# Optimization experiments

Hardware: AMD Instinct MI355X
Metric: run time of the kernel (lower is better)

Reference implementation:

```python
import math
import jax, jax.numpy as jnp
import numpy as np

B, T, C, H = 4, 2048, 1024, 16
D = C // H  # head dim = 64


def setup_inputs() -> dict:
    key = jax.random.key(0)
    ks = jax.random.split(key, 9)
    s = 1.0 / math.sqrt(C)
    return {
        "x": jax.random.normal(ks[0], (B, T, C), jnp.float32),
        "Wq": jax.random.normal(ks[1], (C, C), jnp.float32) * s,
        "bq": jax.random.normal(ks[2], (C,), jnp.float32) * 0.02,
        "Wk": jax.random.normal(ks[3], (C, C), jnp.float32) * s,
        "bk": jax.random.normal(ks[4], (C,), jnp.float32) * 0.02,
        "Wv": jax.random.normal(ks[5], (C, C), jnp.float32) * s,
        "bv": jax.random.normal(ks[6], (C,), jnp.float32) * 0.02,
        "Wo": jax.random.normal(ks[7], (C, C), jnp.float32) * s,
        "bo": jax.random.normal(ks[8], (C,), jnp.float32) * 0.02,
    }


def reference(x, Wq, bq, Wk, bk, Wv, bv, Wo, bo):
    # Projections: (B,T,C) -> (B,H,T,D)
    def heads(y):
        return y.reshape(B, T, H, D).transpose(0, 2, 1, 3)

    q = heads(x @ Wq + bq)
    k = heads(x @ Wk + bk)
    v = heads(x @ Wv + bv)

    scale = 1.0 / math.sqrt(D)
    scores = jnp.einsum("bhqd,bhkd->bhqk", q, k) * scale  # (B,H,T,T)
    causal = jnp.tril(jnp.ones((T, T), dtype=bool))
    scores = jnp.where(causal[None, None], scores, jnp.float32(-jnp.inf))
    att = jax.nn.softmax(scores, axis=-1)

    y = jnp.einsum("bhqk,bhkd->bhqd", att, v)  # (B,H,T,D)
    y = y.transpose(0, 2, 1, 3).reshape(B, T, C)
    return y @ Wo + bo
```

## Files before the change

kernel.cpp:

```cpp
#include <hip/hip_runtime.h>

#define B_ 4
#define T_ 2048
#define C_ 1024
#define H_ 16
#define D_ 64
#define M_ (B_*T_)
#define CR3 3072

typedef unsigned short u16;
typedef __attribute__((ext_vector_type(8))) short short8;
typedef __attribute__((ext_vector_type(8))) unsigned short ushort8_t;
typedef __attribute__((ext_vector_type(4))) unsigned short ushort4_t;
typedef __attribute__((ext_vector_type(4))) float floatx4;
typedef __attribute__((ext_vector_type(16))) float f32x16;
typedef __attribute__((ext_vector_type(4))) unsigned int uint4_t;

__device__ __forceinline__ u16 f2bf(float f) {
  union { float f; unsigned u; } v; v.f = f;
  unsigned r = v.u + 0x7fffu + ((v.u >> 16) & 1u);
  return (u16)(r >> 16);
}

__device__ __forceinline__ void gload16(const void* g, void* l) {
  __builtin_amdgcn_global_load_lds((__attribute__((address_space(1))) void*)(g),
                                   (__attribute__((address_space(3))) void*)(l),
                                   16, 0, 0);
}

__device__ __forceinline__ unsigned cvtpk(float lo, float hi) {
  unsigned r;
  asm("v_cvt_pk_bf16_f32 %0, %1, %2" : "=v"(r) : "v"(lo), "v"(hi));
  return r;
}

__device__ __forceinline__ void pl32swap(unsigned &a, unsigned &b) {
  asm volatile("v_permlane32_swap_b32 %0, %1" : "+v"(a), "+v"(b));
}

#define MFMA32(a, b, c) __builtin_amdgcn_mfma_f32_32x32x16_bf16(a, b, c, 0, 0, 0)
#define MFMA16(a, b, c) __builtin_amdgcn_mfma_f32_16x16x32_bf16(a, b, c, 0, 0, 0)

__global__ __launch_bounds__(256) void convx_k(const float* __restrict__ x,
                                               u16* __restrict__ o) {
  int i = (blockIdx.x * 256 + threadIdx.x) * 4;
  floatx4 v = *(const floatx4*)(x + i);
  ushort4_t r;
#pragma unroll
  for (int j = 0; j < 4; ++j) r[j] = f2bf(v[j]);
  *(ushort4_t*)(o + i) = r;
}

__global__ __launch_bounds__(256) void wconv_k(const float* __restrict__ W0,
                                               const float* __restrict__ W1,
                                               const float* __restrict__ W2,
                                               const float* __restrict__ W3,
                                               u16* __restrict__ WT) {
  __shared__ float tile[64][65];
  const float* W = blockIdx.z == 0 ? W0 : blockIdx.z == 1 ? W1 : blockIdx.z == 2 ? W2 : W3;
  const float sc = blockIdx.z == 0 ? 0.125f * 1.44269504f : 1.0f;
  u16* Wt = WT + (size_t)blockIdx.z * (C_ * C_);
  int k0 = blockIdx.x * 64, n0 = blockIdx.y * 64;
  int t = threadIdx.x;
  int r = t >> 2, c0 = (t & 3) * 16;
#pragma unroll
  for (int j = 0; j < 4; ++j) {
    floatx4 v = *(const floatx4*)(W + (size_t)(k0 + r) * C_ + n0 + c0 + j * 4);
#pragma unroll
    for (int jj = 0; jj < 4; ++jj) tile[r][c0 + j * 4 + jj] = v[jj];
  }
  __syncthreads();
  ushort8_t o0, o1;
#pragma unroll
  for (int j = 0; j < 8; ++j) o0[j] = f2bf(tile[c0 + j][r] * sc);
#pragma unroll
  for (int j = 0; j < 8; ++j) o1[j] = f2bf(tile[c0 + 8 + j][r] * sc);
  *(ushort8_t*)(Wt + (size_t)(n0 + r) * C_ + k0 + c0) = o0;
  *(ushort8_t*)(Wt + (size_t)(n0 + r) * C_ + k0 + c0 + 8) = o1;
}

__global__ __launch_bounds__(256, 2) void gemm8_k(const u16* __restrict__ A,
                                                  const u16* __restrict__ Wt,
                                                  const float* __restrict__ b0,
                                                  const float* __restrict__ b1,
                                                  const float* __restrict__ b2,
                                                  float bsc0,
                                                  u16* __restrict__ Cout) {
  __shared__ u16 lds3[36864];
  const int tid = threadIdx.x;
  const int lane = tid & 63, wn = tid >> 6;
  const int l15 = lane & 15, g = lane >> 4;

  const int bid = blockIdx.x;
  const int swz = (bid & 7) * 96 + (bid >> 3);
  const int bn = swz >> 6, bm = swz & 63;
  const int m0 = bm * 128, n0 = bn * 256;

  const int srow = tid >> 2;
  const int scol = ((tid & 3) ^ ((srow >> 1) & 3)) * 8;
  const u16* gA = A  + (size_t)(m0 + srow) * 1024 + scol;
  const u16* gB = Wt + (size_t)(n0 + srow) * 1024 + scol;

#define STAGE(KT) do { \
    u16* s_ = lds3 + ((KT) % 3) * 12288; \
    gload16(gA + (KT) * 32,                      s_ + tid * 8); \
    gload16(gA + (size_t)64 * 1024 + (KT) * 32,  s_ + 2048 + tid * 8); \
    gload16(gB + (KT) * 32,                      s_ + 4096 + tid * 8); \
    gload16(gB + (size_t)64 * 1024 + (KT) * 32,  s_ + 6144 + tid * 8); \
    gload16(gB + (size_t)128 * 1024 + (KT) * 32, s_ + 8192 + tid * 8); \
    gload16(gB + (size_t)192 * 1024 + (KT) * 32, s_ + 10240 + tid * 8); \
  } while (0)

  floatx4 acc[8][4] = {};

  STAGE(0);
  STAGE(1);

  for (int kt = 0; kt < 32; ++kt) {
    if (kt < 31) asm volatile("s_waitcnt vmcnt(6)" ::: "memory");
    else         asm volatile("s_waitcnt vmcnt(0)" ::: "memory");
    __builtin_amdgcn_s_barrier();
    __builtin_amdgcn_sched_barrier(0);
    if (kt < 30) STAGE(kt + 2);

    const u16* Ab = lds3 + (kt % 3) * 12288;
    const u16* Bb = Ab + 4096;
    short8 af[8], bf[4];
#pragma unroll
    for (int mi = 0; mi < 8; ++mi) {
      int ra = mi * 16 + l15;
      af[mi] = *(const short8*)(Ab + ra * 32 + ((g ^ ((ra >> 1) & 3)) << 3));
    }
#pragma unroll
    for (int ni = 0; ni < 4; ++ni) {
      int rb = wn * 64 + ni * 16 + l15;
      bf[ni] = *(const short8*)(Bb + rb * 32 + ((g ^ ((rb >> 1) & 3)) << 3));
    }
    __builtin_amdgcn_s_setprio(1);
#pragma unroll
    for (int mi = 0; mi < 8; ++mi)
#pragma unroll
      for (int ni = 0; ni < 4; ++ni)
        acc[mi][ni] = MFMA16(af[mi], bf[ni], acc[mi][ni]);
    __builtin_amdgcn_s_setprio(0);
  }

#pragma unroll
  for (int mi = 0; mi < 8; ++mi) {
    int row = m0 + mi * 16 + g * 4;
#pragma unroll
    for (int ni = 0; ni < 4; ++ni) {
      int col = n0 + wn * 64 + ni * 16 + l15;
      int seg = col >> 10;
      const float* bp = seg == 0 ? b0 : seg == 1 ? b1 : b2;
      float bv = bp[col & 1023] * (seg == 0 ? bsc0 : 1.0f);
#pragma unroll
      for (int i = 0; i < 4; ++i)
        Cout[(size_t)(row + i) * CR3 + col] = f2bf(acc[mi][ni][i] + bv);
    }
  }
}

template <int OUTF32>
__global__ __launch_bounds__(256, 2) void gemm_k(const u16* __restrict__ A,
                                                 int astride,
                                                 const u16* __restrict__ Wt,
                                                 const float* __restrict__ b0,
                                                 void* __restrict__ Cout, int ostride) {
  __shared__ u16 As[128 * 32];
  __shared__ u16 Bs[128 * 32];
  const int tid = threadIdx.x;
  const int w = tid >> 6, lane = tid & 63;
  const int wr = (w >> 1) * 64, wc = (w & 1) * 64;
  const int l15 = lane & 15, g = lane >> 4;
  const int m0 = blockIdx.x * 128, n0 = blockIdx.y * 128;

  floatx4 acc[4][4] = {};

  const int srow = tid >> 2;
  const int scol = ((tid & 3) ^ ((srow >> 1) & 3)) * 8;
  const u16* ga = A + (size_t)(m0 + srow) * astride + scol;
  const u16* gb = Wt + (size_t)(n0 + srow) * C_ + scol;
  u16* lA = As + tid * 8;
  u16* lB = Bs + tid * 8;

  for (int kt = 0; kt < C_; kt += 32) {
    gload16(ga + kt, lA);
    gload16(ga + kt + (size_t)64 * astride, lA + 64 * 32);
    gload16(gb + kt, lB);
    gload16(gb + kt + (size_t)64 * C_, lB + 64 * 32);
    asm volatile("s_waitcnt vmcnt(0)" ::: "memory");
    __syncthreads();
    short8 af[4], bf[4];
#pragma unroll
    for (int i = 0; i < 4; ++i) {
      int ra = wr + i * 16 + l15;
      af[i] = *(const short8*)(As + ra * 32 + ((g ^ ((ra >> 1) & 3)) << 3));
    }
#pragma unroll
    for (int i = 0; i < 4; ++i) {
      int rb = wc + i * 16 + l15;
      bf[i] = *(const short8*)(Bs + rb * 32 + ((g ^ ((rb >> 1) & 3)) << 3));
    }
#pragma unroll
    for (int mi = 0; mi < 4; ++mi)
#pragma unroll
      for (int ni = 0; ni < 4; ++ni)
        acc[mi][ni] = MFMA16(af[mi], bf[ni], acc[mi][ni]);
    __syncthreads();
  }
#pragma unroll
  for (int mi = 0; mi < 4; ++mi) {
    int row = m0 + wr + mi * 16 + g * 4;
#pragma unroll
    for (int ni = 0; ni < 4; ++ni) {
      int col = n0 + wc + ni * 16 + l15;
      float bv = b0[col];
#pragma unroll
      for (int i = 0; i < 4; ++i) {
        float v = acc[mi][ni][i] + bv;
        if (OUTF32)
          ((float*)Cout)[(size_t)(row + i) * ostride + col] = v;
        else
          ((u16*)Cout)[(size_t)(row + i) * ostride + col] = f2bf(v);
      }
    }
  }
}

__global__ __launch_bounds__(256, 2) void attn_k(const u16* __restrict__ QKV,
                                                 u16* __restrict__ Yg) {
  __shared__ u16 Ks[2][64 * 64];
  __shared__ u16 Vt[2][64 * 64];

  const int tid = threadIdx.x;
  const int w = tid >> 6, lane = tid & 63;
  const int qi = lane & 31, h = lane >> 5;

  const int lid = blockIdx.x;
  const int a4 = lid >> 6;
  const int gq = a4 >> 2, iq = a4 & 3;
  const int jt = gq == 0 ? 15 - 2 * iq : gq == 1 ? 2 * iq : gq == 2 ? 14 - 2 * iq : 1 + 2 * iq;
  const int bh = lid & 63;
  const int nt = 2 * jt + 2;

  const size_t baseQ = (size_t)(bh >> 4) * T_ * CR3 + (size_t)(bh & 15) * D_;
  const size_t baseY = (size_t)(bh >> 4) * T_ * C_ + (size_t)(bh & 15) * D_;
  const u16* Kg = QKV + baseQ + 1024;
  const u16* Vg = QKV + baseQ + 2048;

  const int srow = tid >> 3, schunk = tid & 7;
  const int sgcol = (schunk ^ (srow & 7)) * 8;
  const u16* Kgr = Kg + (size_t)srow * CR3 + sgcol;
  const u16* Vgr = Vg + (size_t)srow * CR3 + schunk * 8;

  const int qw0 = 128 * jt + 32 * w;
  const int q_abs = qw0 + qi;

  short8 qf0, qf1, qf2, qf3;
  {
    const u16* Qr = QKV + baseQ + (size_t)q_abs * CR3 + 8 * h;
    qf0 = *(const short8*)(Qr);      qf1 = *(const short8*)(Qr + 16);
    qf2 = *(const short8*)(Qr + 32); qf3 = *(const short8*)(Qr + 48);
  }

  ushort8_t va, vbr;
  gload16(Kgr, &Ks[0][tid * 8]);
  gload16(Kgr + (size_t)32 * CR3, &Ks[0][2048 + tid * 8]);
  va = *(const ushort8_t*)(Vgr);
  vbr = *(const ushort8_t*)(Vgr + (size_t)32 * CR3);

  f32x16 y0 = {}, y1 = {};
  float l_run = 0.f;
  const float M0 = 13.0f;

  for (int t = 0; t < nt; ++t) {
    const int kv0 = t * 64;
    u16* Kb = Ks[t & 1];
    u16* Vb = Vt[t & 1];
    asm volatile("s_waitcnt vmcnt(0)" ::: "memory");
    {
      char* vbp = (char*)Vb;
#pragma unroll
      for (int j = 0; j < 8; ++j) {
        int d = schunk * 8 + j;
        int sl = ((schunk ^ j) & 7) << 4;
        *(u16*)(vbp + d * 128 + ((2 * srow) ^ sl)) = va[j];
        *(u16*)(vbp + d * 128 + ((2 * (srow + 32)) ^ sl)) = vbr[j];
      }
    }
    __syncthreads();
    if (t + 1 < nt) {
      int nkv = (t + 1) * 64;
      u16* dst = Ks[(t + 1) & 1];
      gload16(Kgr + (size_t)nkv * CR3, dst + tid * 8);
      gload16(Kgr + (size_t)(nkv + 32) * CR3, dst + 2048 + tid * 8);
      va = *(const ushort8_t*)(Vgr + (size_t)nkv * CR3);
      vbr = *(const ushort8_t*)(Vgr + (size_t)(nkv + 32) * CR3);
    }

    if (kv0 <= qw0 + 31) {
      f32x16 s0 = {}, s1 = {};
      {
        const int swq = (qi & 7) << 4;
        const char* kr0 = (const char*)Kb + qi * 128;
        const char* kr1 = (const char*)Kb + (qi + 32) * 128;
        short8 k0, k1;
        k0 = *(const short8*)(kr0 + ((16 * h) ^ swq));
        k1 = *(const short8*)(kr1 + ((16 * h) ^ swq));
        s0 = MFMA32(k0, qf0, s0); s1 = MFMA32(k1, qf0, s1);
        k0 = *(const short8*)(kr0 + ((32 + 16 * h) ^ swq));
        k1 = *(const short8*)(kr1 + ((32 + 16 * h) ^ swq));
        s0 = MFMA32(k0, qf1, s0); s1 = MFMA32(k1, qf1, s1);
        k0 = *(const short8*)(kr0 + ((64 + 16 * h) ^ swq));
        k1 = *(const short8*)(kr1 + ((64 + 16 * h) ^ swq));
        s0 = MFMA32(k0, qf2, s0); s1 = MFMA32(k1, qf2, s1);
        k0 = *(const short8*)(kr0 + ((96 + 16 * h) ^ swq));
        k1 = *(const short8*)(kr1 + ((96 + 16 * h) ^ swq));
        s0 = MFMA32(k0, qf3, s0); s1 = MFMA32(k1, qf3, s1);
      }
      if (kv0 + 63 > qw0) {
#pragma unroll
        for (int r = 0; r < 16; ++r) {
          int kvq = (r & 3) + 8 * (r >> 2) + 4 * h;
          if (kv0 + kvq > q_abs) s0[r] = -1e30f;
          if (kv0 + 32 + kvq > q_abs) s1[r] = -1e30f;
        }
      }
#pragma unroll
      for (int r = 0; r < 16; ++r) s0[r] = __builtin_amdgcn_exp2f(s0[r] - M0);
#pragma unroll
      for (int r = 0; r < 16; ++r) s1[r] = __builtin_amdgcn_exp2f(s1[r] - M0);
      {
        float a8[8];
#pragma unroll
        for (int r = 0; r < 8; ++r) a8[r] = (s0[r] + s0[r + 8]) + (s1[r] + s1[r + 8]);
#pragma unroll
        for (int r = 0; r < 4; ++r) a8[r] += a8[r + 4];
        l_run += (a8[0] + a8[1]) + (a8[2] + a8[3]);
      }
      unsigned pw[16];
      {
        unsigned a0, b0, a1, b1;
        a0 = cvtpk(s0[0], s0[1]);  b0 = cvtpk(s0[4], s0[5]);  pl32swap(a0, b0);
        a1 = cvtpk(s0[2], s0[3]);  b1 = cvtpk(s0[6], s0[7]);  pl32swap(a1, b1);
        pw[0] = a0; pw[1] = a1; pw[2] = b0; pw[3] = b1;
        a0 = cvtpk(s0[8], s0[9]);  b0 = cvtpk(s0[12], s0[13]); pl32swap(a0, b0);
        a1 = cvtpk(s0[10], s0[11]); b1 = cvtpk(s0[14], s0[15]); pl32swap(a1, b1);
        pw[4] = a0; pw[5] = a1; pw[6] = b0; pw[7] = b1;
        a0 = cvtpk(s1[0], s1[1]);  b0 = cvtpk(s1[4], s1[5]);  pl32swap(a0, b0);
        a1 = cvtpk(s1[2], s1[3]);  b1 = cvtpk(s1[6], s1[7]);  pl32swap(a1, b1);
        pw[8] = a0; pw[9] = a1; pw[10] = b0; pw[11] = b1;
        a0 = cvtpk(s1[8], s1[9]);  b0 = cvtpk(s1[12], s1[13]); pl32swap(a0, b0);
        a1 = cvtpk(s1[10], s1[11]); b1 = cvtpk(s1[14], s1[15]); pl32swap(a1, b1);
        pw[12] = a0; pw[13] = a1; pw[14] = b0; pw[15] = b1;
      }
      {
        const char* vb0 = (const char*)Vb + qi * 128;
        const char* vb1 = (const char*)Vb + (qi + 32) * 128;
        const int sx0 = (((qi >> 3) ^ qi) & 7) << 4;
        const int sx1 = sx0 ^ 0x40;
#pragma unroll
        for (int c = 0; c < 4; ++c) {
          int cb = 32 * c + 16 * h;
          uint4_t pt = {pw[c * 4 + 0], pw[c * 4 + 1], pw[c * 4 + 2], pw[c * 4 + 3]};
          short8 pa = __builtin_bit_cast(short8, pt);
          short8 v0 = *(const short8*)(vb0 + (cb ^ sx0));
          short8 v1 = *(const short8*)(vb1 + (cb ^ sx1));
          y0 = MFMA32(pa, v0, y0);
          y1 = MFMA32(pa, v1, y1);
        }
      }
    }
  }

  l_run += __shfl_xor(l_run, 32);
  float linv = 1.0f / l_run;
#pragma unroll
  for (int r = 0; r < 16; ++r) {
    int qp = (r & 3) + 8 * (r >> 2) + 4 * h;
    float lv = __shfl(linv, qp);
    size_t row = baseY + (size_t)(qw0 + qp) * C_;
    Yg[row + qi] = f2bf(y0[r] * lv);
    Yg[row + 32 + qi] = f2bf(y1[r] * lv);
  }
}

extern "C" void kernel_launch(void* const* d_in, const int* in_sizes, int n_in,
                              void* d_out, int out_size, void* d_ws, size_t ws_size,
                              hipStream_t stream) {
  const float* x  = (const float*)d_in[0];
  const float* Wq = (const float*)d_in[1];
  const float* bq = (const float*)d_in[2];
  const float* Wk = (const float*)d_in[3];
  const float* bk = (const float*)d_in[4];
  const float* Wv = (const float*)d_in[5];
  const float* bv = (const float*)d_in[6];
  const float* Wo = (const float*)d_in[7];
  const float* bo = (const float*)d_in[8];
  float* out = (float*)d_out;

  char* ws = (char*)d_ws;
  u16* xb   = (u16*)ws;
  u16* WT   = (u16*)(ws + (size_t)16777216);
  u16* QKVb = (u16*)(ws + (size_t)25165824);
  u16* Yb = xb;

  convx_k<<<dim3(M_ * C_ / 1024), 256, 0, stream>>>(x, xb);
  wconv_k<<<dim3(16, 16, 4), 256, 0, stream>>>(Wq, Wk, Wv, Wo, WT);
  gemm8_k<<<dim3(768), 256, 0, stream>>>(xb, WT, bq, bk, bv, 0.125f * 1.44269504f, QKVb);
  attn_k<<<dim3(1024), 256, 0, stream>>>(QKVb, Yb);
  gemm_k<1><<<dim3(64, 8), 256, 0, stream>>>(Yb, C_, WT + (size_t)3 * 1048576, bo, out, C_);
}
```

Baseline: 163.7 us.

## Restructure QKV GEMM into 256x256 tiles with 8-wave phased pipeline

The QKV projection GEMM moves from 128x256 tiles with 4 waves and a 3-stage ring buffer to 256x256 tiles with 8 waves, K-steps of 64, and a double-buffered LDS schedule. Global loads are interleaved into eight compute phases per iteration, each bracketed by barriers. Larger tiles increase operand reuse and halve the grid. The cost is 128KB of LDS per block, which limits occupancy, plus more barriers. The attention kernel also wraps its MFMA pairs in s_setprio to favour matrix issue.

```diff
diff --git a/kernel.cpp b/kernel.cpp
--- a/kernel.cpp
+++ b/kernel.cpp
@@ -79,75 +79,94 @@
   *(ushort8_t*)(Wt + (size_t)(n0 + r) * C_ + k0 + c0 + 8) = o1;
 }
 
-__global__ __launch_bounds__(256, 2) void gemm8_k(const u16* __restrict__ A,
+__global__ __launch_bounds__(512, 2) void gemm8_k(const u16* __restrict__ A,
                                                   const u16* __restrict__ Wt,
                                                   const float* __restrict__ b0,
                                                   const float* __restrict__ b1,
                                                   const float* __restrict__ b2,
                                                   float bsc0,
                                                   u16* __restrict__ Cout) {
-  __shared__ u16 lds3[36864];
+  __shared__ u16 lds[65536];
   const int tid = threadIdx.x;
-  const int lane = tid & 63, wn = tid >> 6;
+  const int lane = tid & 63, w = tid >> 6;
+  const int wm = w >> 2, wn = w & 3;
   const int l15 = lane & 15, g = lane >> 4;
 
   const int bid = blockIdx.x;
-  const int swz = (bid & 7) * 96 + (bid >> 3);
-  const int bn = swz >> 6, bm = swz & 63;
-  const int m0 = bm * 128, n0 = bn * 256;
-
-  const int srow = tid >> 2;
-  const int scol = ((tid & 3) ^ ((srow >> 1) & 3)) * 8;
-  const u16* gA = A  + (size_t)(m0 + srow) * 1024 + scol;
-  const u16* gB = Wt + (size_t)(n0 + srow) * 1024 + scol;
-
-#define STAGE(KT) do { \
-    u16* s_ = lds3 + ((KT) % 3) * 12288; \
-    gload16(gA + (KT) * 32,                      s_ + tid * 8); \
-    gload16(gA + (size_t)64 * 1024 + (KT) * 32,  s_ + 2048 + tid * 8); \
-    gload16(gB + (KT) * 32,                      s_ + 4096 + tid * 8); \
-    gload16(gB + (size_t)64 * 1024 + (KT) * 32,  s_ + 6144 + tid * 8); \
-    gload16(gB + (size_t)128 * 1024 + (KT) * 32, s_ + 8192 + tid * 8); \
-    gload16(gB + (size_t)192 * 1024 + (KT) * 32, s_ + 10240 + tid * 8); \
+  const int swz = (bid & 7) * 48 + (bid >> 3);
+  const int bn = swz >> 5, bm = swz & 31;
+  const int m0 = bm * 256, n0 = bn * 256;
+
+  const int srow = tid >> 3;
+  const int scol = ((tid & 7) ^ (srow & 7)) * 8;
+  const u16* gAsrc = A  + (size_t)(m0 + srow) * 1024 + scol;
+  const u16* gBsrc = Wt + (size_t)(n0 + srow) * 1024 + scol;
+
+#define SQA(DD, Q, KT) gload16(gAsrc + (size_t)(Q) * 65536 + (size_t)(KT) * 64, \
+                               lds + (DD) * 32768 + (Q) * 4096 + tid * 8)
+#define SQB(DD, Q, KT) gload16(gBsrc + (size_t)(Q) * 65536 + (size_t)(KT) * 64, \
+                               lds + (DD) * 32768 + 16384 + (Q) * 4096 + tid * 8)
+
+  floatx4 acc[8][4] = {};
+  short8 bk0[4], bk1[4];
+
+#define PHASE(DD, MH, KS, READB, BKREG, STG, VM) do {                       \
+    short8 af_[4];                                                          \
+    _Pragma("unroll") for (int mi = 0; mi < 4; ++mi) {                      \
+      int ar_ = wm * 128 + (MH) * 64 + mi * 16 + l15;                       \
+      af_[mi] = *(const short8*)(lds + (DD) * 32768 + ar_ * 64 +            \
+                                 ((((KS) * 4 + g) ^ (ar_ & 7)) << 3));      \
+    }                                                                       \
+    if (READB) {                                                            \
+      _Pragma("unroll") for (int ni = 0; ni < 4; ++ni) {                    \
+        int br_ = wn * 64 + ni * 16 + l15;                                  \
+        BKREG[ni] = *(const short8*)(lds + (DD) * 32768 + 16384 + br_ * 64 +\
+                                     ((((KS) * 4 + g) ^ (br_ & 7)) << 3));  \
+      }                                                                     \
+    }                                                                       \
+    STG;                                                                    \
+    VM;                                                                     \
+    __builtin_amdgcn_s_barrier();                                           \
+    asm volatile("s_waitcnt lgkmcnt(0)" ::: "memory");                      \
+    __builtin_amdgcn_sched_barrier(0);                                      \
+    __builtin_amdgcn_s_setprio(1);                                          \
+    _Pragma("unroll") for (int mi = 0; mi < 4; ++mi)                        \
+      _Pragma("unroll") for (int ni = 0; ni < 4; ++ni)                      \
+        acc[(MH) * 4 + mi][ni] = MFMA16(af_[mi], BKREG[ni],                 \
+                                        acc[(MH) * 4 + mi][ni]);            \
+    __builtin_amdgcn_s_setprio(0);                                          \
+    __builtin_amdgcn_sched_barrier(0);                                      \
+    __builtin_amdgcn_s_barrier();                                           \
   } while (0)
 
-  floatx4 acc[8][4] = {};
-
-  STAGE(0);
-  STAGE(1);
-
-  for (int kt = 0; kt < 32; ++kt) {
-    if (kt < 31) asm volatile("s_waitcnt vmcnt(6)" ::: "memory");
-    else         asm volatile("s_waitcnt vmcnt(0)" ::: "memory");
-    __builtin_amdgcn_s_barrier();
-    __builtin_amdgcn_sched_barrier(0);
-    if (kt < 30) STAGE(kt + 2);
-
-    const u16* Ab = lds3 + (kt % 3) * 12288;
-    const u16* Bb = Ab + 4096;
-    short8 af[8], bf[4];
-#pragma unroll
-    for (int mi = 0; mi < 8; ++mi) {
-      int ra = mi * 16 + l15;
-      af[mi] = *(const short8*)(Ab + ra * 32 + ((g ^ ((ra >> 1) & 3)) << 3));
-    }
-#pragma unroll
-    for (int ni = 0; ni < 4; ++ni) {
-      int rb = wn * 64 + ni * 16 + l15;
-      bf[ni] = *(const short8*)(Bb + rb * 32 + ((g ^ ((rb >> 1) & 3)) << 3));
-    }
-    __builtin_amdgcn_s_setprio(1);
-#pragma unroll
-    for (int mi = 0; mi < 8; ++mi)
-#pragma unroll
-      for (int ni = 0; ni < 4; ++ni)
-        acc[mi][ni] = MFMA16(af[mi], bf[ni], acc[mi][ni]);
-    __builtin_amdgcn_s_setprio(0);
-  }
-
-#pragma unroll
-  for (int mi = 0; mi < 8; ++mi) {
-    int row = m0 + mi * 16 + g * 4;
+#define VM4 asm volatile("s_waitcnt vmcnt(4)" ::: "memory")
+#define VM0 asm volatile("s_waitcnt vmcnt(0)" ::: "memory")
+#define NOP ((void)0)
+
+  SQA(0, 0, 0); SQA(0, 1, 0); SQA(0, 2, 0); SQA(0, 3, 0);
+  SQB(0, 0, 0); SQB(0, 1, 0); SQB(0, 2, 0); SQB(0, 3, 0);
+  SQB(1, 0, 1); SQB(1, 1, 1); SQB(1, 2, 1); SQB(1, 3, 1);
+  VM4;
+  __builtin_amdgcn_s_barrier();
+
+  for (int i = 0; i < 8; ++i) {
+    const int t1 = 2 * i + 1, T2 = 2 * i + 2, T3 = 2 * i + 3;
+    const bool st = (i < 7);
+    PHASE(0, 0, 0, 1, bk0, { SQA(1, 0, t1); SQA(1, 1, t1); }, NOP);
+    PHASE(0, 0, 1, 1, bk1, { SQA(1, 2, t1); SQA(1, 3, t1); }, NOP);
+    PHASE(0, 1, 0, 0, bk0, { if (st) { SQB(0, 0, T2); SQB(0, 1, T2); } }, NOP);
+    if (st) { PHASE(0, 1, 1, 0, bk1, { SQB(0, 2, T2); SQB(0, 3, T2); }, VM4); }
+    else    { PHASE(0, 1, 1, 0, bk1, NOP, VM0); }
+    PHASE(1, 0, 0, 1, bk0, { if (st) { SQA(0, 0, T2); SQA(0, 1, T2); } }, NOP);
+    PHASE(1, 0, 1, 1, bk1, { if (st) { SQA(0, 2, T2); SQA(0, 3, T2); } }, NOP);
+    PHASE(1, 1, 0, 0, bk0, { if (st) { SQB(1, 0, T3); SQB(1, 1, T3); } }, NOP);
+    if (st) { PHASE(1, 1, 1, 0, bk1, { SQB(1, 2, T3); SQB(1, 3, T3); }, VM4); }
+    else    { PHASE(1, 1, 1, 0, bk1, NOP, VM0); }
+  }
+
+#pragma unroll
+  for (int mi8 = 0; mi8 < 8; ++mi8) {
+    int row = m0 + wm * 128 + mi8 * 16 + g * 4;
 #pragma unroll
     for (int ni = 0; ni < 4; ++ni) {
       int col = n0 + wn * 64 + ni * 16 + l15;
@@ -156,7 +175,7 @@
       float bv = bp[col & 1023] * (seg == 0 ? bsc0 : 1.0f);
 #pragma unroll
       for (int i = 0; i < 4; ++i)
-        Cout[(size_t)(row + i) * CR3 + col] = f2bf(acc[mi][ni][i] + bv);
+        Cout[(size_t)(row + i) * CR3 + col] = f2bf(acc[mi8][ni][i] + bv);
     }
   }
 }
@@ -308,16 +327,24 @@
         short8 k0, k1;
         k0 = *(const short8*)(kr0 + ((16 * h) ^ swq));
         k1 = *(const short8*)(kr1 + ((16 * h) ^ swq));
+        __builtin_amdgcn_s_setprio(1);
         s0 = MFMA32(k0, qf0, s0); s1 = MFMA32(k1, qf0, s1);
+        __builtin_amdgcn_s_setprio(0);
         k0 = *(const short8*)(kr0 + ((32 + 16 * h) ^ swq));
         k1 = *(const short8*)(kr1 + ((32 + 16 * h) ^ swq));
+        __builtin_amdgcn_s_setprio(1);
         s0 = MFMA32(k0, qf1, s0); s1 = MFMA32(k1, qf1, s1);
+        __builtin_amdgcn_s_setprio(0);
         k0 = *(const short8*)(kr0 + ((64 + 16 * h) ^ swq));
         k1 = *(const short8*)(kr1 + ((64 + 16 * h) ^ swq));
+        __builtin_amdgcn_s_setprio(1);
         s0 = MFMA32(k0, qf2, s0); s1 = MFMA32(k1, qf2, s1);
+        __builtin_amdgcn_s_setprio(0);
         k0 = *(const short8*)(kr0 + ((96 + 16 * h) ^ swq));
         k1 = *(const short8*)(kr1 + ((96 + 16 * h) ^ swq));
+        __builtin_amdgcn_s_setprio(1);
         s0 = MFMA32(k0, qf3, s0); s1 = MFMA32(k1, qf3, s1);
+        __builtin_amdgcn_s_setprio(0);
       }
       if (kv0 + 63 > qw0) {
 #pragma unroll
@@ -367,8 +394,10 @@
           short8 pa = __builtin_bit_cast(short8, pt);
           short8 v0 = *(const short8*)(vb0 + (cb ^ sx0));
           short8 v1 = *(const short8*)(vb1 + (cb ^ sx1));
+          __builtin_amdgcn_s_setprio(1);
           y0 = MFMA32(pa, v0, y0);
           y1 = MFMA32(pa, v1, y1);
+          __builtin_amdgcn_s_setprio(0);
         }
       }
     }
@@ -408,7 +437,7 @@
 
   convx_k<<<dim3(M_ * C_ / 1024), 256, 0, stream>>>(x, xb);
   wconv_k<<<dim3(16, 16, 4), 256, 0, stream>>>(Wq, Wk, Wv, Wo, WT);
-  gemm8_k<<<dim3(768), 256, 0, stream>>>(xb, WT, bq, bk, bv, 0.125f * 1.44269504f, QKVb);
+  gemm8_k<<<dim3(384), 512, 0, stream>>>(xb, WT, bq, bk, bv, 0.125f * 1.44269504f, QKVb);
   attn_k<<<dim3(1024), 256, 0, stream>>>(QKVb, Yb);
   gemm_k<1><<<dim3(64, 8), 256, 0, stream>>>(Yb, C_, WT + (size_t)3 * 1048576, bo, out, C_);
 }
```

After: 163.2 us. About the same (-0.3%).

## Rewrite output projection GEMM with 3-stage LDS pipeline and larger tiles

Applied to the files above, without the earlier changes.

Replaces the generic output-projection GEMM with a specialised kernel that uses 128x256 tiles, a triple-buffered LDS pipeline with partial vmcnt waits, and a swizzled block order for L2 locality. Each wave now computes 8x4 MFMA tiles, sharing the A tile across all waves. The intent is to overlap global loads with MFMA work and drop the per-iteration double barrier of the old kernel. It also adds s_setprio around MFMA groups in the attention kernel to favour matrix issue. The larger accumulator and 72KB of LDS may limit occupancy.

```diff
diff --git a/kernel.cpp b/kernel.cpp
--- a/kernel.cpp
+++ b/kernel.cpp
@@ -161,69 +161,79 @@
   }
 }
 
-template <int OUTF32>
-__global__ __launch_bounds__(256, 2) void gemm_k(const u16* __restrict__ A,
-                                                 int astride,
-                                                 const u16* __restrict__ Wt,
-                                                 const float* __restrict__ b0,
-                                                 void* __restrict__ Cout, int ostride) {
-  __shared__ u16 As[128 * 32];
-  __shared__ u16 Bs[128 * 32];
+__global__ __launch_bounds__(256, 2) void gemmO_k(const u16* __restrict__ A,
+                                                  const u16* __restrict__ Wt,
+                                                  const float* __restrict__ b0,
+                                                  float* __restrict__ Cout) {
+  __shared__ u16 lds3[36864];
   const int tid = threadIdx.x;
-  const int w = tid >> 6, lane = tid & 63;
-  const int wr = (w >> 1) * 64, wc = (w & 1) * 64;
+  const int lane = tid & 63, wn = tid >> 6;
   const int l15 = lane & 15, g = lane >> 4;
-  const int m0 = blockIdx.x * 128, n0 = blockIdx.y * 128;
-
-  floatx4 acc[4][4] = {};
+
+  const int bid = blockIdx.x;
+  const int swz = (bid & 7) * 32 + (bid >> 3);
+  const int bn = swz >> 6, bm = swz & 63;
+  const int m0 = bm * 128, n0 = bn * 256;
 
   const int srow = tid >> 2;
   const int scol = ((tid & 3) ^ ((srow >> 1) & 3)) * 8;
-  const u16* ga = A + (size_t)(m0 + srow) * astride + scol;
-  const u16* gb = Wt + (size_t)(n0 + srow) * C_ + scol;
-  u16* lA = As + tid * 8;
-  u16* lB = Bs + tid * 8;
-
-  for (int kt = 0; kt < C_; kt += 32) {
-    gload16(ga + kt, lA);
-    gload16(ga + kt + (size_t)64 * astride, lA + 64 * 32);
-    gload16(gb + kt, lB);
-    gload16(gb + kt + (size_t)64 * C_, lB + 64 * 32);
-    asm volatile("s_waitcnt vmcnt(0)" ::: "memory");
-    __syncthreads();
-    short8 af[4], bf[4];
-#pragma unroll
-    for (int i = 0; i < 4; ++i) {
-      int ra = wr + i * 16 + l15;
-      af[i] = *(const short8*)(As + ra * 32 + ((g ^ ((ra >> 1) & 3)) << 3));
-    }
-#pragma unroll
-    for (int i = 0; i < 4; ++i) {
-      int rb = wc + i * 16 + l15;
-      bf[i] = *(const short8*)(Bs + rb * 32 + ((g ^ ((rb >> 1) & 3)) << 3));
-    }
-#pragma unroll
-    for (int mi = 0; mi < 4; ++mi)
+  const u16* gA = A  + (size_t)(m0 + srow) * 1024 + scol;
+  const u16* gB = Wt + (size_t)(n0 + srow) * 1024 + scol;
+
+#define STAGEO(KT) do { \
+    u16* s_ = lds3 + ((KT) % 3) * 12288; \
+    gload16(gA + (KT) * 32,                      s_ + tid * 8); \
+    gload16(gA + (size_t)64 * 1024 + (KT) * 32,  s_ + 2048 + tid * 8); \
+    gload16(gB + (KT) * 32,                      s_ + 4096 + tid * 8); \
+    gload16(gB + (size_t)64 * 1024 + (KT) * 32,  s_ + 6144 + tid * 8); \
+    gload16(gB + (size_t)128 * 1024 + (KT) * 32, s_ + 8192 + tid * 8); \
+    gload16(gB + (size_t)192 * 1024 + (KT) * 32, s_ + 10240 + tid * 8); \
+  } while (0)
+
+  floatx4 acc[8][4] = {};
+
+  STAGEO(0);
+  STAGEO(1);
+
+  for (int kt = 0; kt < 32; ++kt) {
+    if (kt < 31) asm volatile("s_waitcnt vmcnt(6)" ::: "memory");
+    else         asm volatile("s_waitcnt vmcnt(0)" ::: "memory");
+    __builtin_amdgcn_s_barrier();
+    __builtin_amdgcn_sched_barrier(0);
+    if (kt < 30) STAGEO(kt + 2);
+
+    const u16* Ab = lds3 + (kt % 3) * 12288;
+    const u16* Bb = Ab + 4096;
+    short8 af[8], bf[4];
+#pragma unroll
+    for (int mi = 0; mi < 8; ++mi) {
+      int ra = mi * 16 + l15;
+      af[mi] = *(const short8*)(Ab + ra * 32 + ((g ^ ((ra >> 1) & 3)) << 3));
+    }
+#pragma unroll
+    for (int ni = 0; ni < 4; ++ni) {
+      int rb = wn * 64 + ni * 16 + l15;
+      bf[ni] = *(const short8*)(Bb + rb * 32 + ((g ^ ((rb >> 1) & 3)) << 3));
+    }
+    __builtin_amdgcn_s_setprio(1);
+#pragma unroll
+    for (int mi = 0; mi < 8; ++mi)
 #pragma unroll
       for (int ni = 0; ni < 4; ++ni)
         acc[mi][ni] = MFMA16(af[mi], bf[ni], acc[mi][ni]);
-    __syncthreads();
-  }
-#pragma unroll
-  for (int mi = 0; mi < 4; ++mi) {
-    int row = m0 + wr + mi * 16 + g * 4;
+    __builtin_amdgcn_s_setprio(0);
+  }
+
+#pragma unroll
+  for (int mi = 0; mi < 8; ++mi) {
+    int row = m0 + mi * 16 + g * 4;
 #pragma unroll
     for (int ni = 0; ni < 4; ++ni) {
-      int col = n0 + wc + ni * 16 + l15;
+      int col = n0 + wn * 64 + ni * 16 + l15;
       float bv = b0[col];
 #pragma unroll
-      for (int i = 0; i < 4; ++i) {
-        float v = acc[mi][ni][i] + bv;
-        if (OUTF32)
-          ((float*)Cout)[(size_t)(row + i) * ostride + col] = v;
-        else
-          ((u16*)Cout)[(size_t)(row + i) * ostride + col] = f2bf(v);
-      }
+      for (int i = 0; i < 4; ++i)
+        Cout[(size_t)(row + i) * 1024 + col] = acc[mi][ni][i] + bv;
     }
   }
 }
@@ -308,16 +318,24 @@
         short8 k0, k1;
         k0 = *(const short8*)(kr0 + ((16 * h) ^ swq));
         k1 = *(const short8*)(kr1 + ((16 * h) ^ swq));
+        __builtin_amdgcn_s_setprio(1);
         s0 = MFMA32(k0, qf0, s0); s1 = MFMA32(k1, qf0, s1);
+        __builtin_amdgcn_s_setprio(0);
         k0 = *(const short8*)(kr0 + ((32 + 16 * h) ^ swq));
         k1 = *(const short8*)(kr1 + ((32 + 16 * h) ^ swq));
+        __builtin_amdgcn_s_setprio(1);
         s0 = MFMA32(k0, qf1, s0); s1 = MFMA32(k1, qf1, s1);
+        __builtin_amdgcn_s_setprio(0);
         k0 = *(const short8*)(kr0 + ((64 + 16 * h) ^ swq));
         k1 = *(const short8*)(kr1 + ((64 + 16 * h) ^ swq));
+        __builtin_amdgcn_s_setprio(1);
         s0 = MFMA32(k0, qf2, s0); s1 = MFMA32(k1, qf2, s1);
+        __builtin_amdgcn_s_setprio(0);
         k0 = *(const short8*)(kr0 + ((96 + 16 * h) ^ swq));
         k1 = *(const short8*)(kr1 + ((96 + 16 * h) ^ swq));
+        __builtin_amdgcn_s_setprio(1);
         s0 = MFMA32(k0, qf3, s0); s1 = MFMA32(k1, qf3, s1);
+        __builtin_amdgcn_s_setprio(0);
       }
       if (kv0 + 63 > qw0) {
 #pragma unroll
@@ -367,8 +385,10 @@
           short8 pa = __builtin_bit_cast(short8, pt);
           short8 v0 = *(const short8*)(vb0 + (cb ^ sx0));
           short8 v1 = *(const short8*)(vb1 + (cb ^ sx1));
+          __builtin_amdgcn_s_setprio(1);
           y0 = MFMA32(pa, v0, y0);
           y1 = MFMA32(pa, v1, y1);
+          __builtin_amdgcn_s_setprio(0);
         }
       }
     }
@@ -410,5 +430,5 @@
   wconv_k<<<dim3(16, 16, 4), 256, 0, stream>>>(Wq, Wk, Wv, Wo, WT);
   gemm8_k<<<dim3(768), 256, 0, stream>>>(xb, WT, bq, bk, bv, 0.125f * 1.44269504f, QKVb);
   attn_k<<<dim3(1024), 256, 0, stream>>>(QKVb, Yb);
-  gemm_k<1><<<dim3(64, 8), 256, 0, stream>>>(Yb, C_, WT + (size_t)3 * 1048576, bo, out, C_);
-}
+  gemmO_k<<<dim3(256), 256, 0, stream>>>(Yb, WT + (size_t)3 * 1048576, bo, out);
+}
```

After: 162.9 us. No clear change (-0.5%).
